# Optimization experiments

Measured on AMD Instinct MI355X. Metric: run time of the kernel, lower is better.

The kernel has to match this reference:

```python
import jax, jax.numpy as jnp
import numpy as np

H8, W8 = 64, 64
H4, W4 = 128, 128
C_LAT, C_HI = 256, 128
N_Q = 1024
ORIG_H, ORIG_W = 512, 512
NUM_ITERS = 4
TEMP = 20.0
DIM = 4 + C_HI + C_LAT        # 388 mixer output dim
IN_DIM = DIM + 3 * 49         # 535 mixer input dim
HID = 512


def _unit(v):
    return v / jnp.sqrt(jnp.maximum(jnp.sum(v * v, axis=-1, keepdims=True), 1e-12))


def setup_inputs() -> dict:
    key = jax.random.key(0)
    ks = jax.random.split(key, 20)
    fg = _unit(jax.random.normal(ks[0], (1, H8, W8, C_LAT), jnp.float32))
    hg = _unit(jax.random.normal(ks[1], (1, H4, W4, C_HI), jnp.float32))
    qf = _unit(jax.random.normal(ks[2], (1, N_Q, C_LAT), jnp.float32))
    hq = _unit(jax.random.normal(ks[3], (1, N_Q, C_HI), jnp.float32))
    p = lambda k, s, sc=0.05: sc * jax.random.normal(k, s, jnp.float32)
    return dict(
        feature_grid=fg, hires_feats_grid=hg, query_feats=qf, hires_query_feats=hq,
        hid1_w=p(ks[4], (16, 1, 3, 3)), hid1_b=jnp.zeros((16,), jnp.float32),
        hid2_w=p(ks[5], (1, 16, 3, 3)), hid2_b=jnp.zeros((1,), jnp.float32),
        hid3_w=p(ks[6], (32, 16, 3, 3)), hid3_b=jnp.zeros((32,), jnp.float32),
        hid4_w=p(ks[7], (32, 16)), hid4_b=jnp.zeros((16,), jnp.float32),
        occ_w=p(ks[8], (16, 2)), occ_b=jnp.zeros((2,), jnp.float32),
        mix_in_w=p(ks[9], (IN_DIM, HID), 0.02), mix_in_b=jnp.zeros((HID,), jnp.float32),
        mix_out_w=p(ks[10], (HID, DIM), 0.02), mix_out_b=jnp.zeros((DIM,), jnp.float32),
    )


def _conv2d(x, w, b, stride, pad):
    y = jax.lax.conv_general_dilated(x, w, (stride, stride), pad,
                                     dimension_numbers=('NCHW', 'OIHW', 'NCHW'))
    return y + b[None, :, None, None]


def _bilinear_sample(grid, coords):
    # grid [H,W,C]; coords [..., 2] as (y, x); edge-clamped bilinear gather.
    H, W = grid.shape[0], grid.shape[1]
    y, x = coords[..., 0], coords[..., 1]
    y0f, x0f = jnp.floor(y), jnp.floor(x)
    wy, wx = (y - y0f)[..., None], (x - x0f)[..., None]
    y0 = jnp.clip(y0f.astype(jnp.int32), 0, H - 1)
    y1 = jnp.clip(y0f.astype(jnp.int32) + 1, 0, H - 1)
    x0 = jnp.clip(x0f.astype(jnp.int32), 0, W - 1)
    x1 = jnp.clip(x0f.astype(jnp.int32) + 1, 0, W - 1)
    g00, g01 = grid[y0, x0], grid[y0, x1]
    g10, g11 = grid[y1, x0], grid[y1, x1]
    return (g00 * (1 - wy) * (1 - wx) + g01 * (1 - wy) * wx
            + g10 * wy * (1 - wx) + g11 * wy * wx)


def _forward(fg, hg, qf, hq, hid1_w, hid1_b, hid2_w, hid2_b, hid3_w, hid3_b,
             hid4_w, hid4_b, occ_w, occ_b, mix_in_w, mix_in_b, mix_out_w, mix_out_b):
    # --- tracks_from_cost_volume ---
    cv = jnp.einsum('bnc,bhwc->bnhw', qf, fg)                 # [1,N,64,64]
    b, n, h, w = cv.shape
    x = cv.reshape(b * n, 1, h, w)
    occ_map = jax.nn.relu(_conv2d(x, hid1_w, hid1_b, 1, 'SAME'))   # [bn,16,h,w]
    pmap = _conv2d(occ_map, hid2_w, hid2_b, 1, 'SAME').reshape(b * n, h * w)
    heat = jax.nn.softmax(pmap * TEMP, axis=-1).reshape(b * n, h, w)
    ey = jnp.einsum('bhw,h->b', heat, jnp.arange(h, dtype=jnp.float32))
    ex = jnp.einsum('bhw,w->b', heat, jnp.arange(w, dtype=jnp.float32))
    points = jnp.stack([ex * (ORIG_W / w), ey * (ORIG_H / h)], -1).reshape(b, n, 2)
    op = jnp.pad(occ_map, ((0, 0), (0, 0), (0, 2), (0, 2)))
    o3 = jax.nn.relu(_conv2d(op, hid3_w, hid3_b, 2, 'VALID'))
    o3 = o3.mean((-1, -2))                                     # [bn,32]
    o3 = jax.nn.relu(o3 @ hid4_w + hid4_b)
    o3 = (o3 @ occ_w + occ_b).reshape(b, n, 2)
    occ, expd = o3[..., 0], o3[..., 1]

    # --- iterative pips refinement ---
    cy, cx = jnp.meshgrid(jnp.arange(-3, 4), jnp.arange(-3, 4), indexing='ij')
    ctx = jnp.stack([cy, cx], -1).reshape(-1, 2).astype(jnp.float32)   # [49,2] (dy,dx)
    fg_avg = fg.reshape(1, H8 // 2, 2, W8 // 2, 2, C_LAT).mean((2, 4))
    pyramid = [hg, fg, fg_avg]
    feats = jnp.concatenate([hq, qf], -1)                      # [1,N,384]
    pos = points
    for it in range(NUM_ITERS):
        if it == 0:
            queries = [hq[0], qf[0], qf[0]]
        else:
            queries = [feats[0, :, :C_HI], feats[0, :, C_HI:], feats[0, :, C_HI:]]
        corrs = []
        for grid, q in zip(pyramid, queries):
            gh, gw = grid.shape[1], grid.shape[2]
            scale = jnp.array([gw / ORIG_W, gh / ORIG_H], jnp.float32)
            c = (pos[0] * scale)[:, ::-1]                      # (x,y)->(y,x), [N,2]
            coords2 = c[:, None, :] + ctx[None]                # [N,49,2]
            nb = _bilinear_sample(grid[0], coords2)            # [N,49,C]
            corrs.append(jnp.einsum('nsc,nc->ns', nb, q))
        corrs = jnp.concatenate(corrs, -1)[None]               # [1,N,147]
        mlp_in = jnp.concatenate([jnp.zeros_like(pos), occ[..., None],
                                  expd[..., None], feats, corrs], -1)
        res = jax.nn.gelu(mlp_in @ mix_in_w + mix_in_b) @ mix_out_w + mix_out_b
        pos = pos + res[..., :2]
        occ = occ + res[..., 2]
        expd = expd + res[..., 3]
        feats = feats + res[..., 4:]
    return jnp.concatenate([pos, occ[..., None], expd[..., None]], -1)  # [1,N,4]


def reference(feature_grid, hires_feats_grid, query_feats, hires_query_feats,
              hid1_w, hid1_b, hid2_w, hid2_b, hid3_w, hid3_b, hid4_w, hid4_b,
              occ_w, occ_b, mix_in_w, mix_in_b, mix_out_w, mix_out_b):
    return _forward(feature_grid, hires_feats_grid, query_feats, hires_query_feats,
                    hid1_w, hid1_b, hid2_w, hid2_b, hid3_w, hid3_b, hid4_w, hid4_b,
                    occ_w, occ_b, mix_in_w, mix_in_b, mix_out_w, mix_out_b)
```

## Files before the change

kernel.cpp:

```cpp
#include <hip/hip_runtime.h>
#include <hip/hip_bf16.h>
#include <math.h>


#define NQ 1024
#define TEMPF 20.0f
#define DIMV 388
#define INDIM 535
#define KPAD 544
#define HID 512

#define WS_CV      0
#define WS_FGAVG   (WS_CV + NQ*4096)
#define WS_POS     (WS_FGAVG + 262144)
#define WS_OCC     (WS_POS + NQ*2)
#define WS_EXPD    (WS_OCC + NQ)
#define WS_FEATS   (WS_EXPD + NQ)
#define WS_MLPIN   (WS_FEATS + NQ*384)
#define WS_HIDDEN  (WS_MLPIN + NQ*KPAD)
#define WS_W3B     (WS_HIDDEN + NQ*HID)
#define WS_PART    (WS_MLPIN + 278528)
#define WS_SUM3    WS_HIDDEN
#define WS_WIT     WS_CV
#define WS_WOT     (WS_CV + 139264)

#define OP 72

typedef __attribute__((ext_vector_type(8))) short bf16x8;
typedef __attribute__((ext_vector_type(4))) float f32x4;

__global__ __launch_bounds__(256) void k_prep(
    const float* __restrict__ fg, const float* __restrict__ qf,
    const float* __restrict__ hq, const float* __restrict__ w3,
    float* __restrict__ ws) {
  int i = blockIdx.x * 256 + threadIdx.x;
  if (i < 262144) {
    int c = i & 255, ox = (i >> 8) & 31, oy = i >> 13;
    const float* b = fg + (((oy * 2) * 64 + ox * 2) << 8) + c;
    ws[WS_FGAVG + i] = 0.25f * (b[0] + b[256] + b[16384] + b[16384 + 256]);
  } else if (i < 262144 + 393216) {
    int j = i - 262144;
    int n = j / 384, c = j - n * 384;
    ws[WS_FEATS + j] = (c < 128) ? hq[n * 128 + c] : qf[n * 256 + c - 128];
  } else if (i < 262144 + 393216 + 5120) {
    int j = i - (262144 + 393216);
    int e = j & 7, qd = (j >> 3) & 3, nl = (j >> 5) & 15;
    int nt = (j >> 9) & 1, kt = j >> 10;
    int k = kt * 32 + qd * 8 + e;
    int ic = k & 15, tap = k >> 4;
    int oc = nt * 16 + nl;
    float v = (tap < 9) ? w3[(oc * 16 + ic) * 9 + tap] : 0.f;
    ((__hip_bfloat16*)(ws + WS_W3B))[j] = __float2bfloat16(v);
  } else if (i < 262144 + 393216 + 5120 + 524288) {
    int j = i - (262144 + 393216 + 5120);
    ws[WS_SUM3 + j] = 0.f;
  }
}

__global__ __launch_bounds__(256) void k_cvt(
    const float* __restrict__ wi, const float* __restrict__ wo,
    float* __restrict__ ws) {
  int i = blockIdx.x * 256 + threadIdx.x;
  __hip_bfloat16* WIT = (__hip_bfloat16*)(ws + WS_WIT);
  __hip_bfloat16* WOT = (__hip_bfloat16*)(ws + WS_WOT);
  if (i < 278528) {
    int n = i / KPAD, k = i - n * KPAD;
    float v = (k < INDIM) ? wi[k * HID + n] : 0.f;
    WIT[i] = __float2bfloat16(v);
  } else if (i < 278528 + 229376) {
    int j = i - 278528;
    int n = j >> 9, k = j & 511;
    float v = (n < DIMV) ? wo[k * DIMV + n] : 0.f;
    WOT[j] = __float2bfloat16(v);
  }
}

__global__ __launch_bounds__(256) void k_cv(
    const float* __restrict__ qf, const float* __restrict__ fg,
    float* __restrict__ ws) {
  __shared__ float As[32][68];
  __shared__ float Bs[32][68];
  int t = threadIdx.x;
  int tx = t & 15, ty = t >> 4;
  int p0 = blockIdx.x * 64, m0 = blockIdx.y * 64;
  float acc[4][4] = {{0.f,0.f,0.f,0.f},{0.f,0.f,0.f,0.f},
                     {0.f,0.f,0.f,0.f},{0.f,0.f,0.f,0.f}};
  for (int k0 = 0; k0 < 256; k0 += 32) {
#pragma unroll
    for (int j = 0; j < 8; j++) {
      int idx = t + 256 * j;
      int kk = idx & 31, mm = idx >> 5;
      As[kk][mm] = qf[(m0 + mm) * 256 + k0 + kk];
      Bs[kk][mm] = fg[(p0 + mm) * 256 + k0 + kk];
    }
    __syncthreads();
#pragma unroll
    for (int k = 0; k < 32; k++) {
      float4 a = *(const float4*)&As[k][ty * 4];
      float4 b = *(const float4*)&Bs[k][tx * 4];
      float av[4] = {a.x, a.y, a.z, a.w};
      float bv[4] = {b.x, b.y, b.z, b.w};
#pragma unroll
      for (int i = 0; i < 4; i++)
#pragma unroll
        for (int jj = 0; jj < 4; jj++) acc[i][jj] += av[i] * bv[jj];
    }
    __syncthreads();
  }
#pragma unroll
  for (int i = 0; i < 4; i++) {
    float4 v = make_float4(acc[i][0], acc[i][1], acc[i][2], acc[i][3]);
    *(float4*)&ws[WS_CV + (m0 + ty * 4 + i) * 4096 + p0 + tx * 4] = v;
  }
}

__global__ __launch_bounds__(256, 4) void k_head_stripe(
    const float* __restrict__ h1w, const float* __restrict__ h1b,
    const float* __restrict__ h2w, const float* __restrict__ h2b,
    const float* __restrict__ h3b, float* __restrict__ ws) {
  __shared__ float cvs[8 * 66];
  __shared__ float occ[6 * 16 * OP];

  const int bx = blockIdx.x;
  const int q = bx >> 4, st = bx & 15;
  const int y0 = st * 4;
  const int t = threadIdx.x;
  const int wv = t >> 6, lane = t & 63;
  const int role = (wv + bx) & 3;
  const float* cv = ws + WS_CV + q * 4096;

  {
    float4 z = make_float4(0.f, 0.f, 0.f, 0.f);
    float4* o4 = (float4*)occ;
    for (int i = t; i < 6 * 16 * OP / 4; i += 256) o4[i] = z;
  }
#pragma unroll
  for (int j = 0; j < 2; j++) {
    int i = t + 256 * j;
    int lr = i >> 6, x = i & 63;
    int g = y0 - 2 + lr;
    cvs[lr * 66 + x + 1] = (g >= 0 && g < 64) ? cv[g * 64 + x] : 0.f;
  }
  if (t < 16) cvs[(t >> 1) * 66 + (t & 1) * 65] = 0.f;
  __syncthreads();

  {
    const int x = lane;
    const int chg = wv * 4;
    float w1r[4][9], b1r[4];
#pragma unroll
    for (int k = 0; k < 4; k++) {
      b1r[k] = h1b[chg + k];
#pragma unroll
      for (int j = 0; j < 9; j++) w1r[k][j] = h1w[(chg + k) * 9 + j];
    }
    for (int r = 0; r < 6; r++) {
      int yo = y0 - 1 + r;
      if (yo >= 0 && yo <= 63) {
        float p[9];
#pragma unroll
        for (int ky = 0; ky < 3; ky++) {
          const float* cp = &cvs[(r + ky) * 66 + x];
          p[3 * ky] = cp[0]; p[3 * ky + 1] = cp[1]; p[3 * ky + 2] = cp[2];
        }
#pragma unroll
        for (int k = 0; k < 4; k++) {
          float a = b1r[k];
#pragma unroll
          for (int j = 0; j < 9; j++) a += w1r[k][j] * p[j];
          occ[(r * 16 + chg + k) * OP + x + 4] = fmaxf(a, 0.f);
        }
      }
    }
  }
  __syncthreads();

  if (role == 1 || role == 2) {
    const __hip_bfloat16* W3B = (const __hip_bfloat16*)(ws + WS_W3B);
    const int oyl = role - 1;
    const int nl = lane & 15;
    const int qd = lane >> 4, qh = qd >> 1, ql = qd & 1;
    f32x4 acc00 = {0.f,0.f,0.f,0.f}, acc01 = {0.f,0.f,0.f,0.f};
    f32x4 acc10 = {0.f,0.f,0.f,0.f}, acc11 = {0.f,0.f,0.f,0.f};
#pragma unroll
    for (int kt = 0; kt < 5; kt++) {
      int tap = kt * 2 + qh;
      int tv = (tap < 9) ? tap : 0;
      int ky = (tv >= 6) ? 2 : ((tv >= 3) ? 1 : 0);
      int kx = tv - 3 * ky;
      const float* ap =
          &occ[((2 * oyl + 1 + ky) * 16 + ql * 8) * OP + 4 + kx + 2 * nl];
      union { bf16x8 v; __hip_bfloat16 h[8]; } a0u, a1u;
      if (tap < 9) {
#pragma unroll
        for (int j = 0; j < 8; j++) {
          a0u.h[j] = __float2bfloat16(ap[j * OP]);
          a1u.h[j] = __float2bfloat16(ap[j * OP + 32]);
        }
      } else {
#pragma unroll
        for (int j = 0; j < 8; j++) {
          a0u.h[j] = __float2bfloat16(0.f);
          a1u.h[j] = __float2bfloat16(0.f);
        }
      }
      bf16x8 b0 = *(const bf16x8*)&W3B[((kt * 2 + 0) * 16 + nl) * 32 + qd * 8];
      bf16x8 b1 = *(const bf16x8*)&W3B[((kt * 2 + 1) * 16 + nl) * 32 + qd * 8];
      acc00 = __builtin_amdgcn_mfma_f32_16x16x32_bf16(a0u.v, b0, acc00, 0, 0, 0);
      acc01 = __builtin_amdgcn_mfma_f32_16x16x32_bf16(a0u.v, b1, acc01, 0, 0, 0);
      acc10 = __builtin_amdgcn_mfma_f32_16x16x32_bf16(a1u.v, b0, acc10, 0, 0, 0);
      acc11 = __builtin_amdgcn_mfma_f32_16x16x32_bf16(a1u.v, b1, acc11, 0, 0, 0);
    }
    float bb0 = h3b[nl], bb1 = h3b[16 + nl];
    float s0 = 0.f, s1 = 0.f;
#pragma unroll
    for (int r = 0; r < 4; r++) {
      s0 += fmaxf(acc00[r] + bb0, 0.f) + fmaxf(acc10[r] + bb0, 0.f);
      s1 += fmaxf(acc01[r] + bb1, 0.f) + fmaxf(acc11[r] + bb1, 0.f);
    }
    s0 += __shfl_xor(s0, 16); s0 += __shfl_xor(s0, 32);
    s1 += __shfl_xor(s1, 16); s1 += __shfl_xor(s1, 32);
    if (lane < 16) {
      atomicAdd(&ws[WS_SUM3 + (q * 16 + st) * 32 + nl], s0);
      atomicAdd(&ws[WS_SUM3 + (q * 16 + st) * 32 + 16 + nl], s1);
    }
  } else {
    const int rl = ((role == 3) ? 2 : 0) + (lane >> 5);
    const int yg = y0 + rl;
    const int x0 = (lane & 31) * 2;
    float pa = 0.f, pb = 0.f;
    for (int ch = 0; ch < 16; ch++) {
#pragma unroll
      for (int ky = 0; ky < 3; ky++) {
        const float* bp = &occ[((rl + ky) * 16 + ch) * OP + x0];
        float f0 = bp[3];
        float2 fm = *(const float2*)(bp + 4);
        float f3 = bp[6];
        float wa = h2w[ch * 9 + 3 * ky], wb = h2w[ch * 9 + 3 * ky + 1],
              wc = h2w[ch * 9 + 3 * ky + 2];
        pa += wa * f0 + wb * fm.x + wc * fm.y;
        pb += wa * fm.x + wb * fm.y + wc * f3;
      }
    }
    float bb = h2b[0];
    float v0 = (pa + bb) * TEMPF, v1 = (pb + bb) * TEMPF;
    float mg = fmaxf(v0, v1);
#pragma unroll
    for (int off = 1; off < 64; off <<= 1) mg = fmaxf(mg, __shfl_xor(mg, off));
    float e0 = __expf(v0 - mg), e1 = __expf(v1 - mg);
    float s = e0 + e1;
    float sx = e0 * (float)x0 + e1 * (float)(x0 + 1);
    float sy = s * (float)yg;
#pragma unroll
    for (int off = 1; off < 64; off <<= 1) {
      s += __shfl_xor(s, off);
      sx += __shfl_xor(sx, off);
      sy += __shfl_xor(sy, off);
    }
    if (lane == 0) {
      int slot = q * 32 + st * 2 + ((role == 3) ? 1 : 0);
      *(float4*)&ws[WS_PART + slot * 4] = make_float4(mg, s, sx, sy);
    }
  }
}

__global__ __launch_bounds__(256) void k_head_merge(
    const float* __restrict__ w4, const float* __restrict__ b4,
    const float* __restrict__ w5, const float* __restrict__ b5,
    float* __restrict__ ws) {
  __shared__ float sums_s[4][32];
  __shared__ float o4s[4][16];
  int t = threadIdx.x, wv = t >> 6, lane = t & 63;
  int q = blockIdx.x * 4 + wv;

  float M = -1e30f, S = 0.f, SX = 0.f, SY = 0.f;
  if (lane < 32) {
    float4 pv = *(const float4*)&ws[WS_PART + (q * 32 + lane) * 4];
    M = pv.x; S = pv.y; SX = pv.z; SY = pv.w;
  }
#pragma unroll
  for (int off = 1; off < 64; off <<= 1) {
    float Mo = __shfl_xor(M, off), So = __shfl_xor(S, off);
    float SXo = __shfl_xor(SX, off), SYo = __shfl_xor(SY, off);
    float Mn = fmaxf(M, Mo);
    float c1 = __expf(M - Mn), c2 = __expf(Mo - Mn);
    S = S * c1 + So * c2; SX = SX * c1 + SXo * c2; SY = SY * c1 + SYo * c2;
    M = Mn;
  }
  if (lane == 0) {
    ws[WS_POS + q * 2 + 0] = (SX / S) * 8.0f;
    ws[WS_POS + q * 2 + 1] = (SY / S) * 8.0f;
  }

  int ch = lane & 31, half = lane >> 5;
  float sm = 0.f;
#pragma unroll
  for (int s8 = 0; s8 < 8; s8++)
    sm += ws[WS_SUM3 + (q * 16 + half * 8 + s8) * 32 + ch];
  sm += __shfl_xor(sm, 32);
  if (lane < 32) sums_s[wv][lane] = sm * (1.f / 1024.f);
  __syncthreads();
  if (lane < 16) {
    float a = b4[lane];
#pragma unroll
    for (int i = 0; i < 32; i++) a += sums_s[wv][i] * w4[i * 16 + lane];
    o4s[wv][lane] = fmaxf(a, 0.f);
  }
  __syncthreads();
  if (lane < 2) {
    float r = b5[lane];
#pragma unroll
    for (int j = 0; j < 16; j++) r += o4s[wv][j] * w5[j * 2 + lane];
    if (lane == 0) ws[WS_OCC + q] = r;
    else           ws[WS_EXPD + q] = r;
  }
}

__global__ __launch_bounds__(256) void k_corr(
    const float* __restrict__ fg, const float* __restrict__ hg,
    float* __restrict__ ws) {
  __shared__ float qs[384];
  __shared__ float dbuf[3][64];
  int t = threadIdx.x;
  int wv = t >> 6, lane = t & 63;
  int cl = lane & 15, sub = lane >> 4;
  int n = blockIdx.x;
  const float* feats = ws + WS_FEATS + n * 384;
  float posx = ws[WS_POS + n * 2 + 0];
  float posy = ws[WS_POS + n * 2 + 1];
  __hip_bfloat16* mi = (__hip_bfloat16*)(ws + WS_MLPIN) + n * KPAD;

  for (int col = t; col < 384; col += 256) {
    float v = feats[col];
    qs[col] = v;
    mi[4 + col] = __float2bfloat16(v);
  }
  if (t < 4) {
    float v = (t == 2) ? ws[WS_OCC + n] : ((t == 3) ? ws[WS_EXPD + n] : 0.f);
    mi[t] = __float2bfloat16(v);
  }
  __syncthreads();

  float4 qh0 = *(const float4*)&qs[cl * 4];
  float4 qh1 = *(const float4*)&qs[64 + cl * 4];
  float4 qq0 = *(const float4*)&qs[128 + cl * 4];
  float4 qq1 = *(const float4*)&qs[192 + cl * 4];
  float4 qq2 = *(const float4*)&qs[256 + cl * 4];
  float4 qq3 = *(const float4*)&qs[320 + cl * 4];

#pragma unroll
  for (int L = 0; L < 3; L++) {
    const float* grid;
    int Hg, Wg;
    float scl;
    if (L == 0)      { grid = hg;             Hg = 128; Wg = 128; scl = 0.25f; }
    else if (L == 1) { grid = fg;             Hg = 64;  Wg = 64;  scl = 0.125f; }
    else             { grid = ws + WS_FGAVG;  Hg = 32;  Wg = 32;  scl = 0.0625f; }
    float cy = posy * scl, cx = posx * scl;
    int iy = (int)floorf(cy), ix = (int)floorf(cx);
#pragma unroll
    for (int g = 0; g < 4; g++) {
      int p = wv * 16 + g * 4 + sub;
      int a = p >> 3, b = p & 7;
      int row = iy + a - 3; row = row < 0 ? 0 : (row > Hg - 1 ? Hg - 1 : row);
      int col = ix + b - 3; col = col < 0 ? 0 : (col > Wg - 1 ? Wg - 1 : col);
      float acc;
      if (L == 0) {
        const float* gp = grid + (row * Wg + col) * 128 + cl * 4;
        float4 g0 = *(const float4*)gp;
        float4 g1 = *(const float4*)(gp + 64);
        acc = g0.x * qh0.x + g0.y * qh0.y + g0.z * qh0.z + g0.w * qh0.w +
              g1.x * qh1.x + g1.y * qh1.y + g1.z * qh1.z + g1.w * qh1.w;
      } else {
        const float* gp = grid + (row * Wg + col) * 256 + cl * 4;
        float4 g0 = *(const float4*)gp;
        float4 g1 = *(const float4*)(gp + 64);
        float4 g2 = *(const float4*)(gp + 128);
        float4 g3 = *(const float4*)(gp + 192);
        acc = g0.x * qq0.x + g0.y * qq0.y + g0.z * qq0.z + g0.w * qq0.w +
              g1.x * qq1.x + g1.y * qq1.y + g1.z * qq1.z + g1.w * qq1.w +
              g2.x * qq2.x + g2.y * qq2.y + g2.z * qq2.z + g2.w * qq2.w +
              g3.x * qq3.x + g3.y * qq3.y + g3.z * qq3.z + g3.w * qq3.w;
      }
      acc += __shfl_xor(acc, 1);
      acc += __shfl_xor(acc, 2);
      acc += __shfl_xor(acc, 4);
      acc += __shfl_xor(acc, 8);
      if (cl == 0) dbuf[L][p] = acc;
    }
  }
  __syncthreads();

  if (t < 147) {
    int L = t / 49, s = t - L * 49;
    int sa = s / 7, sb = s - sa * 7;
    float scl = (L == 0) ? 0.25f : ((L == 1) ? 0.125f : 0.0625f);
    float cy = posy * scl, cx = posx * scl;
    float wy = cy - floorf(cy), wx = cx - floorf(cx);
    int i00 = sa * 8 + sb;
    float d00 = dbuf[L][i00], d01 = dbuf[L][i00 + 1];
    float d10 = dbuf[L][i00 + 8], d11 = dbuf[L][i00 + 9];
    float corr = (1.f - wy) * (1.f - wx) * d00 + (1.f - wy) * wx * d01 +
                 wy * (1.f - wx) * d10 + wy * wx * d11;
    mi[388 + t] = __float2bfloat16(corr);
  }
}

__device__ __forceinline__ float gelu_tanh(float x) {
  float z = 0.7978845608028654f * (x + 0.044715f * x * x * x);
  z = fminf(fmaxf(z, -15.f), 15.f);
  float e = __expf(2.f * z);
  float th = (e - 1.f) / (e + 1.f);
  return 0.5f * x * (1.f + th);
}

__global__ __launch_bounds__(256) void k_mix1(
    const float* __restrict__ bias, float* __restrict__ ws) {
  __shared__ __hip_bfloat16 A_s[32 * 32];
  __shared__ __hip_bfloat16 B_s[64 * 32];
  const int t = threadIdx.x;
  const int wv = t >> 6, lane = t & 63;
  const int wm = wv & 1, wn = wv >> 1;
  const int quad = lane >> 4, nl = lane & 15;
  const int n0 = blockIdx.x * 64, m0 = blockIdx.y * 32;
  const unsigned short* Abf = (const unsigned short*)(ws + WS_MLPIN);
  const unsigned short* WIT = (const unsigned short*)(ws + WS_WIT);
  f32x4 acc0 = {0.f, 0.f, 0.f, 0.f};
  f32x4 acc1 = {0.f, 0.f, 0.f, 0.f};

  for (int k0 = 0; k0 < KPAD; k0 += 32) {
    if (t < 128) {
      int r = t >> 2, c = t & 3;
      *(uint4*)&A_s[r * 32 + c * 8] =
          *(const uint4*)&Abf[(m0 + r) * KPAD + k0 + c * 8];
    }
    {
      int r = t >> 2, c = t & 3;
      *(uint4*)&B_s[r * 32 + c * 8] =
          *(const uint4*)&WIT[(n0 + r) * KPAD + k0 + c * 8];
    }
    __syncthreads();
    bf16x8 a = *(const bf16x8*)&A_s[(16 * wm + nl) * 32 + quad * 8];
    bf16x8 b0 = *(const bf16x8*)&B_s[(32 * wn + nl) * 32 + quad * 8];
    bf16x8 b1 = *(const bf16x8*)&B_s[(32 * wn + 16 + nl) * 32 + quad * 8];
    acc0 = __builtin_amdgcn_mfma_f32_16x16x32_bf16(a, b0, acc0, 0, 0, 0);
    acc1 = __builtin_amdgcn_mfma_f32_16x16x32_bf16(a, b1, acc1, 0, 0, 0);
    __syncthreads();
  }

  __hip_bfloat16* Hd = (__hip_bfloat16*)(ws + WS_HIDDEN);
#pragma unroll
  for (int nt = 0; nt < 2; nt++) {
    int nn = n0 + 32 * wn + nt * 16 + nl;
    float bv = bias[nn];
#pragma unroll
    for (int r = 0; r < 4; r++) {
      int m = m0 + 16 * wm + quad * 4 + r;
      float v = gelu_tanh((nt ? acc1[r] : acc0[r]) + bv);
      Hd[m * HID + nn] = __float2bfloat16(v);
    }
  }
}

__global__ __launch_bounds__(256) void k_mix2(
    const float* __restrict__ bias, float* __restrict__ ws,
    float* __restrict__ out) {
  __shared__ __hip_bfloat16 A_s[32 * 32];
  __shared__ __hip_bfloat16 B_s[64 * 32];
  const int t = threadIdx.x;
  const int wv = t >> 6, lane = t & 63;
  const int wm = wv & 1, wn = wv >> 1;
  const int quad = lane >> 4, nl = lane & 15;
  const int n0 = blockIdx.x * 64, m0 = blockIdx.y * 32;
  const unsigned short* Abf = (const unsigned short*)(ws + WS_HIDDEN);
  const unsigned short* WOT = (const unsigned short*)(ws + WS_WOT);
  f32x4 acc0 = {0.f, 0.f, 0.f, 0.f};
  f32x4 acc1 = {0.f, 0.f, 0.f, 0.f};

  for (int k0 = 0; k0 < HID; k0 += 32) {
    if (t < 128) {
      int r = t >> 2, c = t & 3;
      *(uint4*)&A_s[r * 32 + c * 8] =
          *(const uint4*)&Abf[(m0 + r) * HID + k0 + c * 8];
    }
    {
      int r = t >> 2, c = t & 3;
      *(uint4*)&B_s[r * 32 + c * 8] =
          *(const uint4*)&WOT[(n0 + r) * HID + k0 + c * 8];
    }
    __syncthreads();
    bf16x8 a = *(const bf16x8*)&A_s[(16 * wm + nl) * 32 + quad * 8];
    bf16x8 b0 = *(const bf16x8*)&B_s[(32 * wn + nl) * 32 + quad * 8];
    bf16x8 b1 = *(const bf16x8*)&B_s[(32 * wn + 16 + nl) * 32 + quad * 8];
    acc0 = __builtin_amdgcn_mfma_f32_16x16x32_bf16(a, b0, acc0, 0, 0, 0);
    acc1 = __builtin_amdgcn_mfma_f32_16x16x32_bf16(a, b1, acc1, 0, 0, 0);
    __syncthreads();
  }

#pragma unroll
  for (int nt = 0; nt < 2; nt++) {
    int col = n0 + 32 * wn + nt * 16 + nl;
    if (col >= DIMV) continue;
    float bv = bias[col];
#pragma unroll
    for (int r = 0; r < 4; r++) {
      int m = m0 + 16 * wm + quad * 4 + r;
      float rr = (nt ? acc1[r] : acc0[r]) + bv;
      if (col < 2) {
        float v = ws[WS_POS + m * 2 + col] + rr;
        ws[WS_POS + m * 2 + col] = v;
        out[m * 4 + col] = v;
      } else if (col == 2) {
        float v = ws[WS_OCC + m] + rr;
        ws[WS_OCC + m] = v;
        out[m * 4 + 2] = v;
      } else if (col == 3) {
        float v = ws[WS_EXPD + m] + rr;
        ws[WS_EXPD + m] = v;
        out[m * 4 + 3] = v;
      } else {
        ws[WS_FEATS + m * 384 + (col - 4)] += rr;
      }
    }
  }
}

extern "C" void kernel_launch(void* const* d_in, const int* in_sizes, int n_in,
                              void* d_out, int out_size, void* d_ws, size_t ws_size,
                              hipStream_t stream) {
  const float* fg = (const float*)d_in[0];
  const float* hg = (const float*)d_in[1];
  const float* qf = (const float*)d_in[2];
  const float* hq = (const float*)d_in[3];
  const float* w1 = (const float*)d_in[4];
  const float* b1 = (const float*)d_in[5];
  const float* w2 = (const float*)d_in[6];
  const float* b2 = (const float*)d_in[7];
  const float* w3 = (const float*)d_in[8];
  const float* b3 = (const float*)d_in[9];
  const float* w4 = (const float*)d_in[10];
  const float* b4 = (const float*)d_in[11];
  const float* w5 = (const float*)d_in[12];
  const float* b5 = (const float*)d_in[13];
  const float* wi = (const float*)d_in[14];
  const float* bi = (const float*)d_in[15];
  const float* wo = (const float*)d_in[16];
  const float* bo = (const float*)d_in[17];
  float* ws = (float*)d_ws;
  float* out = (float*)d_out;

  k_prep<<<4628, 256, 0, stream>>>(fg, qf, hq, w3, ws);
  k_cv<<<dim3(64, 16), 256, 0, stream>>>(qf, fg, ws);
  k_head_stripe<<<16384, 256, 0, stream>>>(w1, b1, w2, b2, b3, ws);
  k_head_merge<<<256, 256, 0, stream>>>(w4, b4, w5, b5, ws);
  k_cvt<<<1984, 256, 0, stream>>>(wi, wo, ws);
  for (int it = 0; it < 4; it++) {
    k_corr<<<1024, 256, 0, stream>>>(fg, hg, ws);
    k_mix1<<<dim3(8, 32), 256, 0, stream>>>(bi, ws);
    k_mix2<<<dim3(7, 32), 256, 0, stream>>>(bo, ws, out);
  }
}
```

Baseline: 361.2 us.

## Use bf16 MFMA for cost volume, vectorize conv1, fuse weight convert into merge

Replaces the fp32 SIMT cost-volume GEMM with bf16 MFMA 16x16x32 tiles and converts inputs to bf16 on load. Vectorizes the first head conv so each lane computes four pixels from float4 shared loads, and zeroes only the occupancy borders instead of the whole buffer. Folds the weight transpose/convert kernel into the head merge kernel to save a launch. The bf16 cost volume lowers precision ahead of a softmax with temperature 20.

```diff
diff --git a/kernel.cpp b/kernel.cpp
--- a/kernel.cpp
+++ b/kernel.cpp
@@ -25,6 +25,7 @@
 #define WS_WOT     (WS_CV + 139264)
 
 #define OP 72
+#define CVP 68
 
 typedef __attribute__((ext_vector_type(8))) short bf16x8;
 typedef __attribute__((ext_vector_type(4))) float f32x4;
@@ -57,60 +58,56 @@
   }
 }
 
-__global__ __launch_bounds__(256) void k_cvt(
-    const float* __restrict__ wi, const float* __restrict__ wo,
-    float* __restrict__ ws) {
-  int i = blockIdx.x * 256 + threadIdx.x;
-  __hip_bfloat16* WIT = (__hip_bfloat16*)(ws + WS_WIT);
-  __hip_bfloat16* WOT = (__hip_bfloat16*)(ws + WS_WOT);
-  if (i < 278528) {
-    int n = i / KPAD, k = i - n * KPAD;
-    float v = (k < INDIM) ? wi[k * HID + n] : 0.f;
-    WIT[i] = __float2bfloat16(v);
-  } else if (i < 278528 + 229376) {
-    int j = i - 278528;
-    int n = j >> 9, k = j & 511;
-    float v = (n < DIMV) ? wo[k * DIMV + n] : 0.f;
-    WOT[j] = __float2bfloat16(v);
-  }
-}
-
 __global__ __launch_bounds__(256) void k_cv(
     const float* __restrict__ qf, const float* __restrict__ fg,
     float* __restrict__ ws) {
-  __shared__ float As[32][68];
-  __shared__ float Bs[32][68];
-  int t = threadIdx.x;
-  int tx = t & 15, ty = t >> 4;
-  int p0 = blockIdx.x * 64, m0 = blockIdx.y * 64;
-  float acc[4][4] = {{0.f,0.f,0.f,0.f},{0.f,0.f,0.f,0.f},
-                     {0.f,0.f,0.f,0.f},{0.f,0.f,0.f,0.f}};
+  __shared__ __hip_bfloat16 A_s[32 * 32];
+  __shared__ __hip_bfloat16 B_s[64 * 32];
+  const int t = threadIdx.x;
+  const int wv = t >> 6, lane = t & 63;
+  const int wm = wv & 1, wn = wv >> 1;
+  const int quad = lane >> 4, nl = lane & 15;
+  const int p0 = blockIdx.x * 64, m0 = blockIdx.y * 32;
+  f32x4 acc0 = {0.f, 0.f, 0.f, 0.f};
+  f32x4 acc1 = {0.f, 0.f, 0.f, 0.f};
+
   for (int k0 = 0; k0 < 256; k0 += 32) {
-#pragma unroll
-    for (int j = 0; j < 8; j++) {
-      int idx = t + 256 * j;
-      int kk = idx & 31, mm = idx >> 5;
-      As[kk][mm] = qf[(m0 + mm) * 256 + k0 + kk];
-      Bs[kk][mm] = fg[(p0 + mm) * 256 + k0 + kk];
+    {
+      int r = t >> 3, c = t & 7;
+      float4 v = *(const float4*)&qf[(m0 + r) * 256 + k0 + c * 4];
+      union { __hip_bfloat16 h[4]; uint2 u; } pk;
+      pk.h[0] = __float2bfloat16(v.x); pk.h[1] = __float2bfloat16(v.y);
+      pk.h[2] = __float2bfloat16(v.z); pk.h[3] = __float2bfloat16(v.w);
+      *(uint2*)&A_s[r * 32 + c * 4] = pk.u;
+    }
+    {
+      int r = t >> 2, c = t & 3;
+      const float* src = &fg[(p0 + r) * 256 + k0 + c * 8];
+      float4 v0 = *(const float4*)src;
+      float4 v1 = *(const float4*)(src + 4);
+      union { __hip_bfloat16 h[8]; uint4 u; } pk;
+      pk.h[0] = __float2bfloat16(v0.x); pk.h[1] = __float2bfloat16(v0.y);
+      pk.h[2] = __float2bfloat16(v0.z); pk.h[3] = __float2bfloat16(v0.w);
+      pk.h[4] = __float2bfloat16(v1.x); pk.h[5] = __float2bfloat16(v1.y);
+      pk.h[6] = __float2bfloat16(v1.z); pk.h[7] = __float2bfloat16(v1.w);
+      *(uint4*)&B_s[r * 32 + c * 8] = pk.u;
     }
     __syncthreads();
-#pragma unroll
-    for (int k = 0; k < 32; k++) {
-      float4 a = *(const float4*)&As[k][ty * 4];
-      float4 b = *(const float4*)&Bs[k][tx * 4];
-      float av[4] = {a.x, a.y, a.z, a.w};
-      float bv[4] = {b.x, b.y, b.z, b.w};
-#pragma unroll
-      for (int i = 0; i < 4; i++)
-#pragma unroll
-        for (int jj = 0; jj < 4; jj++) acc[i][jj] += av[i] * bv[jj];
-    }
+    bf16x8 a = *(const bf16x8*)&A_s[(16 * wm + nl) * 32 + quad * 8];
+    bf16x8 b0 = *(const bf16x8*)&B_s[(32 * wn + nl) * 32 + quad * 8];
+    bf16x8 b1 = *(const bf16x8*)&B_s[(32 * wn + 16 + nl) * 32 + quad * 8];
+    acc0 = __builtin_amdgcn_mfma_f32_16x16x32_bf16(a, b0, acc0, 0, 0, 0);
+    acc1 = __builtin_amdgcn_mfma_f32_16x16x32_bf16(a, b1, acc1, 0, 0, 0);
     __syncthreads();
   }
 #pragma unroll
-  for (int i = 0; i < 4; i++) {
-    float4 v = make_float4(acc[i][0], acc[i][1], acc[i][2], acc[i][3]);
-    *(float4*)&ws[WS_CV + (m0 + ty * 4 + i) * 4096 + p0 + tx * 4] = v;
+  for (int nt = 0; nt < 2; nt++) {
+    int n = p0 + 32 * wn + nt * 16 + nl;
+#pragma unroll
+    for (int r = 0; r < 4; r++) {
+      int m = m0 + 16 * wm + quad * 4 + r;
+      ws[WS_CV + m * 4096 + n] = (nt ? acc1[r] : acc0[r]);
+    }
   }
 }
 
@@ -118,7 +115,7 @@
     const float* __restrict__ h1w, const float* __restrict__ h1b,
     const float* __restrict__ h2w, const float* __restrict__ h2b,
     const float* __restrict__ h3b, float* __restrict__ ws) {
-  __shared__ float cvs[8 * 66];
+  __shared__ float cvs[8 * CVP];
   __shared__ float occ[6 * 16 * OP];
 
   const int bx = blockIdx.x;
@@ -129,24 +126,33 @@
   const int role = (wv + bx) & 3;
   const float* cv = ws + WS_CV + q * 4096;
 
-  {
-    float4 z = make_float4(0.f, 0.f, 0.f, 0.f);
-    float4* o4 = (float4*)occ;
-    for (int i = t; i < 6 * 16 * OP / 4; i += 256) o4[i] = z;
+  if (t < 192) {
+    int rc = t >> 1, side = t & 1;
+    *(float4*)&occ[rc * OP + side * 68] = make_float4(0.f, 0.f, 0.f, 0.f);
+  }
+  if (st == 0 || st == 15) {
+    int r = (st == 0) ? 0 : 5;
+    for (int i = t; i < 16 * 18; i += 256)
+      *(float4*)&occ[(r * 16 + (i / 18)) * OP + (i % 18) * 4] =
+          make_float4(0.f, 0.f, 0.f, 0.f);
   }
 #pragma unroll
   for (int j = 0; j < 2; j++) {
     int i = t + 256 * j;
     int lr = i >> 6, x = i & 63;
     int g = y0 - 2 + lr;
-    cvs[lr * 66 + x + 1] = (g >= 0 && g < 64) ? cv[g * 64 + x] : 0.f;
-  }
-  if (t < 16) cvs[(t >> 1) * 66 + (t & 1) * 65] = 0.f;
+    cvs[lr * CVP + x + 1] = (g >= 0 && g < 64) ? cv[g * 64 + x] : 0.f;
+  }
+  if (t < 32) {
+    int rr = t >> 2, c = t & 3;
+    cvs[rr * CVP + ((c == 0) ? 0 : (64 + c))] = 0.f;
+  }
   __syncthreads();
 
   {
-    const int x = lane;
     const int chg = wv * 4;
+    const int xg = lane & 15, rsel = lane >> 4;
+    const int x0 = xg * 4;
     float w1r[4][9], b1r[4];
 #pragma unroll
     for (int k = 0; k < 4; k++) {
@@ -154,21 +160,35 @@
 #pragma unroll
       for (int j = 0; j < 9; j++) w1r[k][j] = h1w[(chg + k) * 9 + j];
     }
-    for (int r = 0; r < 6; r++) {
+#pragma unroll
+    for (int p = 0; p < 2; p++) {
+      int r = p * 4 + rsel;
       int yo = y0 - 1 + r;
-      if (yo >= 0 && yo <= 63) {
-        float p[9];
+      if (r < 6 && yo >= 0 && yo <= 63) {
+        float rb[3][6];
 #pragma unroll
         for (int ky = 0; ky < 3; ky++) {
-          const float* cp = &cvs[(r + ky) * 66 + x];
-          p[3 * ky] = cp[0]; p[3 * ky + 1] = cp[1]; p[3 * ky + 2] = cp[2];
+          const float* cp = &cvs[(r + ky) * CVP + x0];
+          float4 a4 = *(const float4*)cp;
+          float2 b2 = *(const float2*)(cp + 4);
+          rb[ky][0] = a4.x; rb[ky][1] = a4.y; rb[ky][2] = a4.z;
+          rb[ky][3] = a4.w; rb[ky][4] = b2.x; rb[ky][5] = b2.y;
         }
 #pragma unroll
         for (int k = 0; k < 4; k++) {
-          float a = b1r[k];
-#pragma unroll
-          for (int j = 0; j < 9; j++) a += w1r[k][j] * p[j];
-          occ[(r * 16 + chg + k) * OP + x + 4] = fmaxf(a, 0.f);
+          float o[4];
+#pragma unroll
+          for (int px = 0; px < 4; px++) {
+            float a = b1r[k];
+#pragma unroll
+            for (int ky = 0; ky < 3; ky++)
+              a += w1r[k][3 * ky] * rb[ky][px] +
+                   w1r[k][3 * ky + 1] * rb[ky][px + 1] +
+                   w1r[k][3 * ky + 2] * rb[ky][px + 2];
+            o[px] = fmaxf(a, 0.f);
+          }
+          *(float4*)&occ[(r * 16 + chg + k) * OP + x0 + 4] =
+              make_float4(o[0], o[1], o[2], o[3]);
         }
       }
     }
@@ -264,10 +284,28 @@
   }
 }
 
-__global__ __launch_bounds__(256) void k_head_merge(
+__global__ __launch_bounds__(256) void k_merge_cvt(
     const float* __restrict__ w4, const float* __restrict__ b4,
     const float* __restrict__ w5, const float* __restrict__ b5,
+    const float* __restrict__ wi, const float* __restrict__ wo,
     float* __restrict__ ws) {
+  {
+    int i = blockIdx.x * 256 + threadIdx.x;
+    __hip_bfloat16* WIT = (__hip_bfloat16*)(ws + WS_WIT);
+    __hip_bfloat16* WOT = (__hip_bfloat16*)(ws + WS_WOT);
+    if (i < 278528) {
+      int n = i / KPAD, k = i - n * KPAD;
+      float v = (k < INDIM) ? wi[k * HID + n] : 0.f;
+      WIT[i] = __float2bfloat16(v);
+    } else if (i < 278528 + 229376) {
+      int j = i - 278528;
+      int n = j >> 9, k = j & 511;
+      float v = (n < DIMV) ? wo[k * DIMV + n] : 0.f;
+      WOT[j] = __float2bfloat16(v);
+    }
+  }
+  if (blockIdx.x >= 256) return;
+
   __shared__ float sums_s[4][32];
   __shared__ float o4s[4][16];
   int t = threadIdx.x, wv = t >> 6, lane = t & 63;
@@ -550,10 +588,9 @@
   float* out = (float*)d_out;
 
   k_prep<<<4628, 256, 0, stream>>>(fg, qf, hq, w3, ws);
-  k_cv<<<dim3(64, 16), 256, 0, stream>>>(qf, fg, ws);
+  k_cv<<<dim3(64, 32), 256, 0, stream>>>(qf, fg, ws);
   k_head_stripe<<<16384, 256, 0, stream>>>(w1, b1, w2, b2, b3, ws);
-  k_head_merge<<<256, 256, 0, stream>>>(w4, b4, w5, b5, ws);
-  k_cvt<<<1984, 256, 0, stream>>>(wi, wo, ws);
+  k_merge_cvt<<<1984, 256, 0, stream>>>(w4, b4, w5, b5, wi, wo, ws);
   for (int it = 0; it < 4; it++) {
     k_corr<<<1024, 256, 0, stream>>>(fg, hg, ws);
     k_mix1<<<dim3(8, 32), 256, 0, stream>>>(bi, ws);
```

Measured after the change: 340.8 us. -5.7%, faster.
